# Kernel tuning notes

Measured on AMD Instinct MI355X. Metric: run time of the kernel, lower is better.

## Reference

```python
import jax, jax.numpy as jnp
import numpy as np

N, D, CHUNK = 512, 64, 128
NUM_VALID = 448
TEMP = 13.544
RAW_A, RAW_B = 4.0335, 14.0885
SIGMOID_A_MAX = 100.0  # constants.sigmoid_a_max (upper clip on 'a')


def _sigmoid_params():
    # loss_utils.get_sigmoid_parameters: a = clip(elu(raw_a)+1, max=a_max), b = raw_b
    a = jnp.minimum(jax.nn.elu(jnp.float32(RAW_A)) + 1.0, SIGMOID_A_MAX)
    b = jnp.float32(RAW_B)
    return a, b


def setup_inputs() -> dict:
    key = jax.random.key(0)
    X = jax.random.normal(key, (N, D), dtype=jnp.float32)
    mask_1d = jnp.arange(N) < NUM_VALID  # padded tail is invalid
    return {"X": X, "mask_1d": mask_1d}


def reference(X, mask_1d):
    a, b = _sigmoid_params()
    nc = N // CHUNK
    Xc = X.reshape(nc, CHUNK, D)
    rr, cc = jnp.meshgrid(jnp.arange(nc), jnp.arange(nc), indexing="ij")
    pairs = jnp.stack([rr.ravel(), cc.ravel()], axis=-1)  # [nc*nc, 2]

    def block(rc):
        xa = Xc[rc[0]][:, None, None, :]   # [CHUNK,1,1,D]
        xb = Xc[rc[1]][None, :, :, None]   # [1,CHUNK,D,1]
        # probabilistic_distance: -log sigmoid(-a*|x-y| + b) == softplus(a*|x-y| - b)
        d = jax.nn.softplus(a * jnp.abs(xa - xb) - b)  # [CHUNK,CHUNK,D,D]
        return jnp.mean(d, axis=(-1, -2))              # [CHUNK,CHUNK]

    blocks = jax.lax.map(block, pairs)  # sequential over 16 chunk pairs, [nc*nc,CHUNK,CHUNK]
    tsm = blocks.reshape(nc, nc, CHUNK, CHUNK).transpose(0, 2, 1, 3).reshape(N, N)

    mask2d = mask_1d[:, None] & mask_1d[None, :]
    # masked row-softmax over valid entries (== softmax on the [num_valid,num_valid] block)
    logits = jnp.where(mask2d, -tsm / TEMP, jnp.float32(-1e30))
    soft = jax.nn.softmax(logits, axis=-1)
    return jnp.where(mask2d, soft, 0.0)
```

## Files before the change

kernel.cpp:

```cpp
#include <hip/hip_runtime.h>
#include <hip/hip_fp16.h>


#define NTOT 512
#define NV   448
#define DF   64
#define TEMPC 13.544f
#define NG   512
#define TLO  (-6.0f)
#define GH   (12.0f / 512.0f)
#define GINVH (512.0f / 12.0f)

typedef _Float16 h2 __attribute__((ext_vector_type(2)));

__global__ __launch_bounds__(256) void build_kernel(const float* __restrict__ X,
                                                    unsigned int* __restrict__ tabG,
                                                    float2* __restrict__ idxfrac,
                                                    float tpar) {
  const int j = blockIdx.x;
  const int tid = threadIdx.x;
  __shared__ float sy[DF];
  __shared__ float sG[NG + 1];
  if (tid < DF) sy[tid] = X[j * DF + tid];
  __syncthreads();

  for (int k = tid; k <= NG; k += 256) {
    const float v = TLO + (float)k * GH;
    float acc = 0.f;
#pragma unroll 8
    for (int q = 0; q < DF; ++q) {
      const float d = v - sy[q];
      acc += fmaxf(fmaxf(d, -d), tpar);
    }
    sG[k] = acc;
  }
  __syncthreads();

  for (int k = tid; k < NG; k += 256) {
    __half2 h = __floats2half2_rn(sG[k], sG[k + 1] - sG[k]);
    tabG[j * NG + k] = *reinterpret_cast<unsigned int*>(&h);
  }

  if (tid < DF) {
    const float x = X[j * DF + tid];
    const float u = (fminf(fmaxf(x, TLO), 6.0f) - TLO) * GINVH;
    int idx = (int)u;
    idx = idx > (NG - 2) ? (NG - 2) : idx;
    const float frac = u - (float)idx;
    __half2 pf = __floats2half2_rn(1.0f, frac);
    float pf_bits;
    __builtin_memcpy(&pf_bits, &pf, 4);
    idxfrac[j * DF + tid] = make_float2(__int_as_float(idx), pf_bits);
  }
}

__global__ __launch_bounds__(256, 4) void eval_kernel(const unsigned int* __restrict__ tabG,
                                                      const float2* __restrict__ idxfrac,
                                                      float* __restrict__ sums) {
  const int j0 = blockIdx.x * 16;
  const int i0 = blockIdx.y * 16;

  __shared__ unsigned int sTab[16 * 513];
  __shared__ float2 sIF[16][DF];

  const int tid = threadIdx.x;
  for (int e = tid; e < 16 * NG; e += 256) {
    const int r = e >> 9, c = e & (NG - 1);
    sTab[r * 513 + c] = tabG[(j0 + r) * NG + c];
  }
  for (int e = tid; e < 16 * DF; e += 256) {
    const int r = e >> 6, c = e & (DF - 1);
    sIF[r][c] = idxfrac[(i0 + r) * DF + c];
  }
  __syncthreads();

  const int tx = tid & 15, ty = tid >> 4;
  const int tb = tx * 513;
  float acc0 = 0.f, acc1 = 0.f;

#pragma unroll 1
  for (int pc = 0; pc < 4; ++pc) {
    float2 f[16];
#pragma unroll
    for (int k = 0; k < 16; ++k) f[k] = sIF[ty][pc * 16 + k];
#pragma unroll
    for (int k = 0; k < 16; ++k) {
      const int idx = __float_as_int(f[k].x);
      const unsigned int e = sTab[tb + idx];
      h2 ge, pf;
      __builtin_memcpy(&ge, &e, 4);
      __builtin_memcpy(&pf, &f[k].y, 4);
#if __has_builtin(__builtin_amdgcn_fdot2)
      if (k & 1) acc1 = __builtin_amdgcn_fdot2(ge, pf, acc1, false);
      else       acc0 = __builtin_amdgcn_fdot2(ge, pf, acc0, false);
#else
      const float g0 = (float)ge.x, dg = (float)ge.y, fr = (float)pf.y;
      if (k & 1) acc1 += fmaf(fr, dg, g0);
      else       acc0 += fmaf(fr, dg, g0);
#endif
    }
  }
  sums[(i0 + ty) * NTOT + (j0 + tx)] = acc0 + acc1;
}

__global__ __launch_bounds__(256) void softmax_kernel(const float* __restrict__ sums,
                                                      float* __restrict__ Out,
                                                      float scale) {
  const int row = blockIdx.x;
  const int tid = threadIdx.x;
  float* Rp = Out + row * NTOT;
  if (row >= NV) {
    Rp[tid] = 0.f;
    Rp[tid + 256] = 0.f;
    return;
  }
  const float* Sr = sums + row * NTOT;
  const bool v1 = (tid + 256) < NV;
  const float l0 = Sr[tid] * scale;
  const float l1 = v1 ? Sr[tid + 256] * scale : -3.0e38f;

  __shared__ float redm[4], reds[4];
  float m = fmaxf(l0, l1);
#pragma unroll
  for (int o = 32; o; o >>= 1) m = fmaxf(m, __shfl_xor(m, o));
  if ((tid & 63) == 0) redm[tid >> 6] = m;
  __syncthreads();
  m = fmaxf(fmaxf(redm[0], redm[1]), fmaxf(redm[2], redm[3]));

  const float e0 = __builtin_amdgcn_exp2f(l0 - m);
  const float e1 = v1 ? __builtin_amdgcn_exp2f(l1 - m) : 0.f;
  float s = e0 + e1;
#pragma unroll
  for (int o = 32; o; o >>= 1) s += __shfl_xor(s, o);
  if ((tid & 63) == 0) reds[tid >> 6] = s;
  __syncthreads();
  s = (reds[0] + reds[1]) + (reds[2] + reds[3]);

  const float inv = 1.0f / s;
  Rp[tid] = e0 * inv;
  Rp[tid + 256] = v1 ? e1 * inv : 0.f;
}

extern "C" void kernel_launch(void* const* d_in, const int* in_sizes, int n_in,
                              void* d_out, int out_size, void* d_ws, size_t ws_size,
                              hipStream_t stream) {
  (void)in_sizes; (void)n_in; (void)ws_size; (void)out_size;
  const float* X = (const float*)d_in[0];
  float* Out = (float*)d_out;
  char* ws = (char*)d_ws;

  unsigned int* tabG = (unsigned int*)(ws);
  float2* idxfrac    = (float2*)(ws + (1u << 20));
  float* sums        = (float*)(ws + (1u << 20) + (1u << 18));

  const double a = 5.0335;
  const double b = 14.0885;
  const double LOG2E = 1.4426950408889634;
  const float tpar = (float)(b / a);
  const float scale = (float)(-a * LOG2E / (4096.0 * (double)TEMPC));

  build_kernel<<<NV, 256, 0, stream>>>(X, tabG, idxfrac, tpar);
  dim3 grid(NV / 16, NV / 16);
  eval_kernel<<<grid, 256, 0, stream>>>(tabG, idxfrac, sums);
  softmax_kernel<<<NTOT, 256, 0, stream>>>(sums, Out, scale);
}
```

Before: 70.27 us.

## Fuse table build and pairwise evaluation into one kernel with LDS-resident tables

Merges the per-row table construction and the pairwise evaluation into a single kernel. Each block builds tables for 8 columns directly in LDS and then sweeps all rows in chunks of 32, recomputing the index/fraction pairs on the fly. This removes a kernel launch and the global round trip for the table and index arrays. In exchange, the grid shrinks to 56 blocks, so the GPU is far from full, and work per block becomes serial.

```diff
diff --git a/kernel.cpp b/kernel.cpp
--- a/kernel.cpp
+++ b/kernel.cpp
@@ -10,97 +10,108 @@
 #define TLO  (-6.0f)
 #define GH   (12.0f / 512.0f)
 #define GINVH (512.0f / 12.0f)
+#define BJ   8
+#define CI   32
+#define NCH  (NV / CI)
 
 typedef _Float16 h2 __attribute__((ext_vector_type(2)));
 
-__global__ __launch_bounds__(256) void build_kernel(const float* __restrict__ X,
-                                                    unsigned int* __restrict__ tabG,
-                                                    float2* __restrict__ idxfrac,
-                                                    float tpar) {
-  const int j = blockIdx.x;
+__global__ __launch_bounds__(256) void build_eval_kernel(const float* __restrict__ X,
+                                                         float* __restrict__ sums,
+                                                         float tpar) {
+  const int j0 = blockIdx.x * BJ;
   const int tid = threadIdx.x;
-  __shared__ float sy[DF];
-  __shared__ float sG[NG + 1];
-  if (tid < DF) sy[tid] = X[j * DF + tid];
-  __syncthreads();
 
-  for (int k = tid; k <= NG; k += 256) {
-    const float v = TLO + (float)k * GH;
-    float acc = 0.f;
-#pragma unroll 8
-    for (int q = 0; q < DF; ++q) {
-      const float d = v - sy[q];
-      acc += fmaxf(fmaxf(d, -d), tpar);
-    }
-    sG[k] = acc;
+  __shared__ float sy[BJ][DF];
+  __shared__ float sGf[BJ * 513];
+  __shared__ unsigned int sTab[BJ * 513];
+  __shared__ float2 sIF[CI][DF + 1];
+
+  for (int e = tid; e < BJ * DF; e += 256) {
+    const int r = e >> 6, f = e & 63;
+    sy[r][f] = X[(j0 + r) * DF + f];
   }
   __syncthreads();
 
-  for (int k = tid; k < NG; k += 256) {
-    __half2 h = __floats2half2_rn(sG[k], sG[k + 1] - sG[k]);
-    tabG[j * NG + k] = *reinterpret_cast<unsigned int*>(&h);
-  }
-
-  if (tid < DF) {
-    const float x = X[j * DF + tid];
-    const float u = (fminf(fmaxf(x, TLO), 6.0f) - TLO) * GINVH;
-    int idx = (int)u;
-    idx = idx > (NG - 2) ? (NG - 2) : idx;
-    const float frac = u - (float)idx;
-    __half2 pf = __floats2half2_rn(1.0f, frac);
-    float pf_bits;
-    __builtin_memcpy(&pf_bits, &pf, 4);
-    idxfrac[j * DF + tid] = make_float2(__int_as_float(idx), pf_bits);
-  }
-}
-
-__global__ __launch_bounds__(256, 4) void eval_kernel(const unsigned int* __restrict__ tabG,
-                                                      const float2* __restrict__ idxfrac,
-                                                      float* __restrict__ sums) {
-  const int j0 = blockIdx.x * 16;
-  const int i0 = blockIdx.y * 16;
-
-  __shared__ unsigned int sTab[16 * 513];
-  __shared__ float2 sIF[16][DF];
-
-  const int tid = threadIdx.x;
-  for (int e = tid; e < 16 * NG; e += 256) {
-    const int r = e >> 9, c = e & (NG - 1);
-    sTab[r * 513 + c] = tabG[(j0 + r) * NG + c];
-  }
-  for (int e = tid; e < 16 * DF; e += 256) {
-    const int r = e >> 6, c = e & (DF - 1);
-    sIF[r][c] = idxfrac[(i0 + r) * DF + c];
+#pragma unroll 1
+  for (int r = 0; r < BJ; ++r) {
+    for (int k = tid; k < 513; k += 256) {
+      const float v = TLO + (float)k * GH;
+      float acc = 0.f;
+#pragma unroll 16
+      for (int q = 0; q < DF; ++q) {
+        const float d = v - sy[r][q];
+        acc += fmaxf(fmaxf(d, -d), tpar);
+      }
+      sGf[r * 513 + k] = acc;
+    }
   }
   __syncthreads();
 
-  const int tx = tid & 15, ty = tid >> 4;
+  for (int e = tid; e < BJ * NG; e += 256) {
+    const int r = e >> 9, k = e & (NG - 1);
+    const float g0 = sGf[r * 513 + k];
+    __half2 h = __floats2half2_rn(g0, sGf[r * 513 + k + 1] - g0);
+    unsigned int u; __builtin_memcpy(&u, &h, 4);
+    sTab[r * 513 + k] = u;
+  }
+
+  const int tx = tid & 7, ty = tid >> 3;
   const int tb = tx * 513;
-  float acc0 = 0.f, acc1 = 0.f;
+
+  float xr[8];
+#pragma unroll
+  for (int e = 0; e < 8; ++e) {
+    const int a = tid + e * 256;
+    xr[e] = X[(a >> 6) * DF + (a & 63)];
+  }
 
 #pragma unroll 1
-  for (int pc = 0; pc < 4; ++pc) {
-    float2 f[16];
+  for (int c = 0; c < NCH; ++c) {
+    __syncthreads();
 #pragma unroll
-    for (int k = 0; k < 16; ++k) f[k] = sIF[ty][pc * 16 + k];
+    for (int e = 0; e < 8; ++e) {
+      const int a = tid + e * 256;
+      const float u = (fminf(fmaxf(xr[e], TLO), 6.0f) - TLO) * GINVH;
+      int id = (int)u;
+      id = id > (NG - 2) ? (NG - 2) : id;
+      __half2 pf = __floats2half2_rn(1.0f, u - (float)id);
+      float pfb; __builtin_memcpy(&pfb, &pf, 4);
+      sIF[a >> 6][a & 63] = make_float2(__int_as_float(id), pfb);
+    }
+    __syncthreads();
+    if (c + 1 < NCH) {
 #pragma unroll
-    for (int k = 0; k < 16; ++k) {
-      const int idx = __float_as_int(f[k].x);
-      const unsigned int e = sTab[tb + idx];
-      h2 ge, pf;
-      __builtin_memcpy(&ge, &e, 4);
-      __builtin_memcpy(&pf, &f[k].y, 4);
+      for (int e = 0; e < 8; ++e) {
+        const int a = tid + e * 256;
+        xr[e] = X[((c + 1) * CI + (a >> 6)) * DF + (a & 63)];
+      }
+    }
+    float acc0 = 0.f, acc1 = 0.f;
+#pragma unroll 1
+    for (int pc = 0; pc < 4; ++pc) {
+      float2 f16a[16];
+#pragma unroll
+      for (int k = 0; k < 16; ++k) f16a[k] = sIF[ty][pc * 16 + k];
+#pragma unroll
+      for (int k = 0; k < 16; ++k) {
+        const int id = __float_as_int(f16a[k].x);
+        const unsigned int e = sTab[tb + id];
+        h2 ge, pf;
+        __builtin_memcpy(&ge, &e, 4);
+        __builtin_memcpy(&pf, &f16a[k].y, 4);
 #if __has_builtin(__builtin_amdgcn_fdot2)
-      if (k & 1) acc1 = __builtin_amdgcn_fdot2(ge, pf, acc1, false);
-      else       acc0 = __builtin_amdgcn_fdot2(ge, pf, acc0, false);
+        if (k & 1) acc1 = __builtin_amdgcn_fdot2(ge, pf, acc1, false);
+        else       acc0 = __builtin_amdgcn_fdot2(ge, pf, acc0, false);
 #else
-      const float g0 = (float)ge.x, dg = (float)ge.y, fr = (float)pf.y;
-      if (k & 1) acc1 += fmaf(fr, dg, g0);
-      else       acc0 += fmaf(fr, dg, g0);
+        const float g0 = (float)ge.x, dg = (float)ge.y, fr = (float)pf.y;
+        if (k & 1) acc1 += fmaf(fr, dg, g0);
+        else       acc0 += fmaf(fr, dg, g0);
 #endif
+      }
     }
+    sums[(c * CI + ty) * NTOT + (j0 + tx)] = acc0 + acc1;
   }
-  sums[(i0 + ty) * NTOT + (j0 + tx)] = acc0 + acc1;
 }
 
 __global__ __launch_bounds__(256) void softmax_kernel(const float* __restrict__ sums,
@@ -147,11 +158,7 @@
   (void)in_sizes; (void)n_in; (void)ws_size; (void)out_size;
   const float* X = (const float*)d_in[0];
   float* Out = (float*)d_out;
-  char* ws = (char*)d_ws;
-
-  unsigned int* tabG = (unsigned int*)(ws);
-  float2* idxfrac    = (float2*)(ws + (1u << 20));
-  float* sums        = (float*)(ws + (1u << 20) + (1u << 18));
+  float* sums = (float*)d_ws;
 
   const double a = 5.0335;
   const double b = 14.0885;
@@ -159,8 +166,6 @@
   const float tpar = (float)(b / a);
   const float scale = (float)(-a * LOG2E / (4096.0 * (double)TEMPC));
 
-  build_kernel<<<NV, 256, 0, stream>>>(X, tabG, idxfrac, tpar);
-  dim3 grid(NV / 16, NV / 16);
-  eval_kernel<<<grid, 256, 0, stream>>>(tabG, idxfrac, sums);
+  build_eval_kernel<<<NV / BJ, 256, 0, stream>>>(X, sums, tpar);
   softmax_kernel<<<NTOT, 256, 0, stream>>>(sums, Out, scale);
 }
```

New measurement: 93.20 us. +32.6%, slower.
